# Optimization experiments

Hardware: AMD Instinct MI355X
Metric: run time of the kernel (lower is better)

Reference implementation:

```python
import jax, jax.numpy as jnp
import numpy as np

N = 100000
D = 64
E = 1000000


def setup_inputs() -> dict:
    key = jax.random.key(0)
    k_x, k_e, k_w1, k_b1, k_w2, k_b2 = jax.random.split(key, 6)
    x = jax.random.normal(k_x, (N, D), dtype=jnp.float32)
    edge_index = jax.random.randint(k_e, (2, E), 0, N, dtype=jnp.int64)
    # nn.Linear(2D, D): weight [D, 2D], bias [D]
    lim1 = 1.0 / np.sqrt(2 * D)
    W1 = jax.random.uniform(k_w1, (D, 2 * D), dtype=jnp.float32, minval=-lim1, maxval=lim1)
    b1 = jax.random.uniform(k_b1, (D,), dtype=jnp.float32, minval=-lim1, maxval=lim1)
    # nn.Linear(D, 1): weight [1, D], bias [1]
    lim2 = 1.0 / np.sqrt(D)
    W2 = jax.random.uniform(k_w2, (1, D), dtype=jnp.float32, minval=-lim2, maxval=lim2)
    b2 = jax.random.uniform(k_b2, (1,), dtype=jnp.float32, minval=-lim2, maxval=lim2)
    return {"x": x, "edge_index": edge_index, "W1": W1, "b1": b1, "W2": W2, "b2": b2}


def reference(x, edge_index, W1, b1, W2, b2):
    src = edge_index[0]
    dst = edge_index[1]
    # [E, 2D] gathered edge features
    edge_features = jnp.concatenate([x[src], x[dst]], axis=1)
    h = jax.nn.relu(edge_features @ W1.T + b1)  # [E, D]
    out = h @ W2.T + b2                          # [E, 1]
    return out.squeeze(-1)                       # [E]
```

## Files before the change

kernel.cpp:

```cpp
#include <hip/hip_runtime.h>

#define NDIM 64
#define FDIM 128

typedef _Float16 half8 __attribute__((ext_vector_type(8)));
typedef float    float4v __attribute__((ext_vector_type(4)));

__global__ __launch_bounds__(256) void node_gemm_kernel(
    const float* __restrict__ x,
    const float* __restrict__ W1,
    const float* __restrict__ b1,
    _Float16* __restrict__ Yab,
    int N)
{
    const int wave = threadIdx.x >> 6;
    const int lane = threadIdx.x & 63;
    const int c = lane & 15;
    const int g = lane >> 4;

    const int node0 = (blockIdx.x * 4 + wave) * 16;
    if (node0 >= N) return;

    float4v C[8];
    #pragma unroll
    for (int nt = 0; nt < 8; nt++) C[nt] = (float4v){0.f, 0.f, 0.f, 0.f};

    #pragma unroll
    for (int kk = 0; kk < 2; kk++) {
        const float* ap = x + (size_t)(node0 + c) * NDIM + kk * 32 + g * 8;
        float4v a0 = *(const float4v*)ap;
        float4v a1 = *(const float4v*)(ap + 4);
        half8 A;
        A[0] = (_Float16)a0[0]; A[1] = (_Float16)a0[1];
        A[2] = (_Float16)a0[2]; A[3] = (_Float16)a0[3];
        A[4] = (_Float16)a1[0]; A[5] = (_Float16)a1[1];
        A[6] = (_Float16)a1[2]; A[7] = (_Float16)a1[3];

        #pragma unroll
        for (int nt = 0; nt < 8; nt++) {
            const int jj = nt * 16 + c;
            const float* bp = W1 + (size_t)(jj & 63) * FDIM + (jj >> 6) * 64
                              + kk * 32 + g * 8;
            float4v w0 = *(const float4v*)bp;
            float4v w1 = *(const float4v*)(bp + 4);
            half8 B;
            B[0] = (_Float16)w0[0]; B[1] = (_Float16)w0[1];
            B[2] = (_Float16)w0[2]; B[3] = (_Float16)w0[3];
            B[4] = (_Float16)w1[0]; B[5] = (_Float16)w1[1];
            B[6] = (_Float16)w1[2]; B[7] = (_Float16)w1[3];
            C[nt] = __builtin_amdgcn_mfma_f32_16x16x32_f16(A, B, C[nt], 0, 0, 0);
        }
    }

    #pragma unroll
    for (int nt = 0; nt < 8; nt++) {
        const float badd = (nt < 4) ? b1[nt * 16 + c] : 0.f;
        #pragma unroll
        for (int r = 0; r < 4; r++) {
            Yab[(size_t)(node0 + g * 4 + r) * FDIM + nt * 16 + c] =
                (_Float16)(C[nt][r] + badd);
        }
    }
}

__global__ __launch_bounds__(256) void edge_combine_kernel(
    const _Float16* __restrict__ Yab,
    const int* __restrict__ ei,
    const float* __restrict__ W2,
    const float* __restrict__ b2,
    float* __restrict__ out,
    int E)
{
    const int lane = threadIdx.x & 63;
    const int wave = threadIdx.x >> 6;
    const int grp  = lane >> 3;
    const int j8   = lane & 7;

    const long e0 = (long)blockIdx.x * 256 + wave * 64;
    if (e0 >= E) return;

    float4v w2lo = *(const float4v*)(W2 + j8 * 8);
    float4v w2hi = *(const float4v*)(W2 + j8 * 8 + 4);
    const float b2v = b2[0];

    float keep = 0.f;
    #pragma unroll
    for (int t = 0; t < 8; t++) {
        const long e = e0 + t * 8 + grp;
        const int s = ei[e];
        const int d = ei[E + e];
        half8 a = *(const half8*)(Yab + (size_t)s * FDIM + j8 * 8);
        half8 b = *(const half8*)(Yab + (size_t)d * FDIM + 64 + j8 * 8);

        float acc = 0.f;
        #pragma unroll
        for (int u = 0; u < 8; u++) {
            float h = (float)a[u] + (float)b[u];
            h = h > 0.f ? h : 0.f;
            acc = fmaf(u < 4 ? w2lo[u] : w2hi[u - 4], h, acc);
        }
        acc += __shfl_xor(acc, 1, 64);
        acc += __shfl_xor(acc, 2, 64);
        acc += __shfl_xor(acc, 4, 64);
        if (j8 == t) keep = acc;
    }
    out[e0 + j8 * 8 + grp] = keep + b2v;
}

__global__ __launch_bounds__(256) void edge_mlp_fp32_kernel(
    const float* __restrict__ x, const int* __restrict__ ei,
    const float* __restrict__ W1, const float* __restrict__ b1,
    const float* __restrict__ W2, const float* __restrict__ b2,
    float* __restrict__ out, int E)
{
    int e = blockIdx.x * blockDim.x + threadIdx.x;
    if (e >= E) return;
    int s = ei[e];
    int d = ei[E + e];
    const float* xs = x + (size_t)s * NDIM;
    const float* xd = x + (size_t)d * NDIM;
    float acc = b2[0];
    for (int j = 0; j < NDIM; j++) {
        float h = b1[j];
        for (int k = 0; k < NDIM; k++) {
            h += xs[k] * W1[j * FDIM + k] + xd[k] * W1[j * FDIM + 64 + k];
        }
        acc += W2[j] * (h > 0.f ? h : 0.f);
    }
    out[e] = acc;
}

extern "C" void kernel_launch(void* const* d_in, const int* in_sizes, int n_in,
                              void* d_out, int out_size, void* d_ws, size_t ws_size,
                              hipStream_t stream) {
    const float* x  = (const float*)d_in[0];
    const int*   ei = (const int*)d_in[1];
    const float* W1 = (const float*)d_in[2];
    const float* b1 = (const float*)d_in[3];
    const float* W2 = (const float*)d_in[4];
    const float* b2 = (const float*)d_in[5];
    float* out = (float*)d_out;
    const int E = out_size;
    const int N = in_sizes[0] / NDIM;

    const size_t tbl_bytes = (size_t)N * FDIM * sizeof(_Float16);

    if (ws_size >= tbl_bytes && (N % 16) == 0 && (E % 64) == 0) {
        _Float16* Yab = (_Float16*)d_ws;
        const int nblocks = (N + 63) / 64;
        node_gemm_kernel<<<nblocks, 256, 0, stream>>>(x, W1, b1, Yab, N);
        edge_combine_kernel<<<(E + 255) / 256, 256, 0, stream>>>(
            Yab, ei, W2, b2, out, E);
    } else {
        edge_mlp_fp32_kernel<<<(E + 255) / 256, 256, 0, stream>>>(
            x, ei, W1, b1, W2, b2, out, E);
    }
}
```

Baseline: 143.9 us.

## Pre-convert W1 to fp16 combined layout and transpose node GEMM for vector stores

```diff
diff --git a/kernel.cpp b/kernel.cpp
--- a/kernel.cpp
+++ b/kernel.cpp
@@ -3,12 +3,24 @@
 #define NDIM 64
 #define FDIM 128
 
-typedef _Float16 half8 __attribute__((ext_vector_type(8)));
+typedef _Float16 half8  __attribute__((ext_vector_type(8)));
+typedef _Float16 half4v __attribute__((ext_vector_type(4)));
 typedef float    float4v __attribute__((ext_vector_type(4)));
+
+__global__ __launch_bounds__(256) void prep_wcomb_kernel(
+    const float* __restrict__ W1, _Float16* __restrict__ Wcomb)
+{
+    int i = blockIdx.x * blockDim.x + threadIdx.x;
+    if (i >= FDIM * NDIM) return;
+    int j = i >> 6;
+    int k = i & 63;
+    float v = (j < NDIM) ? W1[j * FDIM + k] : W1[(j - NDIM) * FDIM + NDIM + k];
+    Wcomb[i] = (_Float16)v;
+}
 
 __global__ __launch_bounds__(256) void node_gemm_kernel(
     const float* __restrict__ x,
-    const float* __restrict__ W1,
+    const _Float16* __restrict__ Wcomb,
     const float* __restrict__ b1,
     _Float16* __restrict__ Yab,
     int N)
@@ -21,45 +33,42 @@
     const int node0 = (blockIdx.x * 4 + wave) * 16;
     if (node0 >= N) return;
 
+    half8 Bf[2];
+    #pragma unroll
+    for (int kk = 0; kk < 2; kk++) {
+        const float* bp = x + (size_t)(node0 + c) * NDIM + kk * 32 + g * 8;
+        float4v b0 = *(const float4v*)bp;
+        float4v b1v_ = *(const float4v*)(bp + 4);
+        half8 B;
+        B[0] = (_Float16)b0[0]; B[1] = (_Float16)b0[1];
+        B[2] = (_Float16)b0[2]; B[3] = (_Float16)b0[3];
+        B[4] = (_Float16)b1v_[0]; B[5] = (_Float16)b1v_[1];
+        B[6] = (_Float16)b1v_[2]; B[7] = (_Float16)b1v_[3];
+        Bf[kk] = B;
+    }
+
     float4v C[8];
     #pragma unroll
-    for (int nt = 0; nt < 8; nt++) C[nt] = (float4v){0.f, 0.f, 0.f, 0.f};
+    for (int mt = 0; mt < 8; mt++) C[mt] = (float4v){0.f, 0.f, 0.f, 0.f};
 
     #pragma unroll
     for (int kk = 0; kk < 2; kk++) {
-        const float* ap = x + (size_t)(node0 + c) * NDIM + kk * 32 + g * 8;
-        float4v a0 = *(const float4v*)ap;
-        float4v a1 = *(const float4v*)(ap + 4);
-        half8 A;
-        A[0] = (_Float16)a0[0]; A[1] = (_Float16)a0[1];
-        A[2] = (_Float16)a0[2]; A[3] = (_Float16)a0[3];
-        A[4] = (_Float16)a1[0]; A[5] = (_Float16)a1[1];
-        A[6] = (_Float16)a1[2]; A[7] = (_Float16)a1[3];
-
         #pragma unroll
-        for (int nt = 0; nt < 8; nt++) {
-            const int jj = nt * 16 + c;
-            const float* bp = W1 + (size_t)(jj & 63) * FDIM + (jj >> 6) * 64
-                              + kk * 32 + g * 8;
-            float4v w0 = *(const float4v*)bp;
-            float4v w1 = *(const float4v*)(bp + 4);
-            half8 B;
-            B[0] = (_Float16)w0[0]; B[1] = (_Float16)w0[1];
-            B[2] = (_Float16)w0[2]; B[3] = (_Float16)w0[3];
-            B[4] = (_Float16)w1[0]; B[5] = (_Float16)w1[1];
-            B[6] = (_Float16)w1[2]; B[7] = (_Float16)w1[3];
-            C[nt] = __builtin_amdgcn_mfma_f32_16x16x32_f16(A, B, C[nt], 0, 0, 0);
+        for (int mt = 0; mt < 8; mt++) {
+            half8 Af = *(const half8*)(Wcomb + (size_t)(mt * 16 + c) * NDIM
+                                       + kk * 32 + g * 8);
+            C[mt] = __builtin_amdgcn_mfma_f32_16x16x32_f16(Af, Bf[kk], C[mt], 0, 0, 0);
         }
     }
 
     #pragma unroll
-    for (int nt = 0; nt < 8; nt++) {
-        const float badd = (nt < 4) ? b1[nt * 16 + c] : 0.f;
+    for (int mt = 0; mt < 8; mt++) {
+        float4v badd = (float4v){0.f, 0.f, 0.f, 0.f};
+        if (mt < 4) badd = *(const float4v*)(b1 + mt * 16 + g * 4);
+        half4v o;
         #pragma unroll
-        for (int r = 0; r < 4; r++) {
-            Yab[(size_t)(node0 + g * 4 + r) * FDIM + nt * 16 + c] =
-                (_Float16)(C[nt][r] + badd);
-        }
+        for (int r = 0; r < 4; r++) o[r] = (_Float16)(C[mt][r] + badd[r]);
+        *(half4v*)(Yab + (size_t)(node0 + c) * FDIM + mt * 16 + g * 4) = o;
     }
 }
 
@@ -143,12 +152,18 @@
     const int E = out_size;
     const int N = in_sizes[0] / NDIM;
 
-    const size_t tbl_bytes = (size_t)N * FDIM * sizeof(_Float16);
+    const size_t wcomb_bytes = (size_t)FDIM * NDIM * sizeof(_Float16);
+    const size_t tbl_bytes   = (size_t)N * FDIM * sizeof(_Float16);
 
-    if (ws_size >= tbl_bytes && (N % 16) == 0 && (E % 64) == 0) {
-        _Float16* Yab = (_Float16*)d_ws;
+    if (ws_size >= wcomb_bytes + tbl_bytes && (N % 16) == 0 && (E % 64) == 0) {
+        _Float16* Wcomb = (_Float16*)d_ws;
+        _Float16* Yab   = (_Float16*)((char*)d_ws + wcomb_bytes);
+
+        prep_wcomb_kernel<<<(FDIM * NDIM + 255) / 256, 256, 0, stream>>>(W1, Wcomb);
+
         const int nblocks = (N + 63) / 64;
-        node_gemm_kernel<<<nblocks, 256, 0, stream>>>(x, W1, b1, Yab, N);
+        node_gemm_kernel<<<nblocks, 256, 0, stream>>>(x, Wcomb, b1, Yab, N);
+
         edge_combine_kernel<<<(E + 255) / 256, 256, 0, stream>>>(
             Yab, ei, W2, b2, out, E);
     } else {
```

Result: faster. 133.3 us (-7.4%).
